# Kernel tuning notes

Measured on AMD Instinct MI355X. Metric: run time of the kernel, lower is better.

The kernel has to match this reference:

```python
import jax, jax.numpy as jnp
import numpy as np

E, K, H, I = 16, 4, 2048, 1024
B, S = 1, 2048


def setup_inputs() -> dict:
    key = jax.random.key(0)
    ks = jax.random.split(key, 5)
    scale_in = 1.0 / np.sqrt(H)
    scale_mid = 1.0 / np.sqrt(I)
    return {
        "x": jax.random.normal(ks[0], (B, S, H), dtype=jnp.float32),
        "gate_w": jax.random.normal(ks[1], (E, H), dtype=jnp.float32) * scale_in,
        "w1_gate": jax.random.normal(ks[2], (E, I, H), dtype=jnp.float32) * scale_in,
        "w1_up": jax.random.normal(ks[3], (E, I, H), dtype=jnp.float32) * scale_in,
        "w2": jax.random.normal(ks[4], (E, H, I), dtype=jnp.float32) * scale_mid,
        "topk": K,
    }


def reference(x, gate_w, w1_gate, w1_up, w2, topk):
    orig_shape = x.shape
    xt = x.reshape(-1, x.shape[-1])            # [T, H]
    T = xt.shape[0]
    n_exp = gate_w.shape[0]

    # Router: top-k logits, softmax over the selected k (as in the torch code).
    logits = xt @ gate_w.T                      # [T, E]
    topk_vals, topk_ids = jax.lax.top_k(logits, topk)
    topk_w = jax.nn.softmax(topk_vals, axis=-1)  # [T, K]

    # Dense per-token-per-expert combine weight; 0 for unselected experts.
    # Mathematically identical to the gather/scatter-add loop: unselected
    # experts contribute expert_out * 0.
    gate_dense = jnp.zeros((T, n_exp), dtype=xt.dtype)
    gate_dense = gate_dense.at[jnp.arange(T)[:, None], topk_ids].add(topk_w)

    # SwiGLU per expert (dense over experts; weights zero-out unused ones).
    g = jnp.einsum("th,eih->tei", xt, w1_gate)   # [T, E, I]
    u = jnp.einsum("th,eih->tei", xt, w1_up)     # [T, E, I]
    h = jax.nn.silu(g) * u                        # [T, E, I]
    out = jnp.einsum("tei,te,ehi->th", h, gate_dense, w2)  # [T, H]
    return out.reshape(orig_shape)
```

## Files before the change

kernel.cpp:

```cpp
#include <hip/hip_runtime.h>
#include <hip/hip_bf16.h>
#include <stdint.h>

#define NEXP 16
#define KSEL 4
#define HDIM 2048
#define IDIM 1024
#define TTOK 2048
#define MAXTILES 80
#define NTA 8
#define NTB 16
#define MAXBA (MAXTILES * NTA)
#define MAXBB (MAXTILES * NTB)

typedef __attribute__((ext_vector_type(8))) short bf16x8;
typedef __attribute__((ext_vector_type(4))) float f32x4;
typedef __attribute__((ext_vector_type(4))) unsigned int u32x4;
typedef unsigned int u32;

__device__ __forceinline__ uint32_t pack2(float a, float b) {
  __hip_bfloat162 h = __float22bfloat162_rn(float2{a, b});
  uint32_t u;
  __builtin_memcpy(&u, &h, 4);
  return u;
}
__device__ __forceinline__ ushort bf1(float a) {
  __hip_bfloat16 h = __float2bfloat16(a);
  ushort u;
  __builtin_memcpy(&u, &h, 2);
  return u;
}
__device__ __forceinline__ float bf2f(ushort u) {
  uint32_t v = (uint32_t)u << 16;
  float f;
  __builtin_memcpy(&f, &v, 4);
  return f;
}
__device__ __forceinline__ void gload16(const void* g, void* l) {
  __builtin_amdgcn_global_load_lds(
      (const __attribute__((address_space(1))) u32*)g,
      (__attribute__((address_space(3))) u32*)l, 16, 0, 0);
}
__device__ __forceinline__ int swzread(int row, int q) {
  return row * 32 + ((q ^ ((row >> 1) & 3)) << 3);
}

__global__ __launch_bounds__(256) void cvtw_kernel(
    const float* __restrict__ src, ushort* __restrict__ dst, int n8)
{
  const int stride = gridDim.x * 256;
  for (int i = blockIdx.x * 256 + threadIdx.x; i < n8; i += stride) {
    f32x4 a = __builtin_nontemporal_load(((const f32x4*)src) + i * 2);
    f32x4 b = __builtin_nontemporal_load(((const f32x4*)src) + i * 2 + 1);
    uint4 t;
    t.x = pack2(a[0], a[1]); t.y = pack2(a[2], a[3]);
    t.z = pack2(b[0], b[1]); t.w = pack2(b[2], b[3]);
    ((uint4*)dst)[i] = t;
  }
}

__global__ __launch_bounds__(256) void router_kernel(
    const float* __restrict__ x, const float* __restrict__ gw,
    ushort* __restrict__ xb, int* __restrict__ topk_id,
    float* __restrict__ topk_w)
{
  const int wid = threadIdx.x >> 6;
  const int lane = threadIdx.x & 63;
  const int t = blockIdx.x * 4 + wid;
  const float4* x4 = (const float4*)(x + (size_t)t * HDIM);
  const float4* gw4 = (const float4*)gw;
  float acc[NEXP];
#pragma unroll
  for (int e = 0; e < NEXP; ++e) acc[e] = 0.f;
#pragma unroll
  for (int i = 0; i < HDIM / 256; ++i) {
    const int idx = i * 64 + lane;
    float4 xv = x4[idx];
    uint2 xp;
    xp.x = pack2(xv.x, xv.y);
    xp.y = pack2(xv.z, xv.w);
    *(uint2*)(xb + (size_t)t * HDIM + idx * 4) = xp;
#pragma unroll
    for (int e = 0; e < NEXP; ++e) {
      float4 wv = gw4[e * (HDIM / 4) + idx];
      acc[e] += xv.x * wv.x + xv.y * wv.y + xv.z * wv.z + xv.w * wv.w;
    }
  }
#pragma unroll
  for (int e = 0; e < NEXP; ++e) {
#pragma unroll
    for (int off = 32; off >= 1; off >>= 1)
      acc[e] += __shfl_xor(acc[e], off);
  }
  if (lane == 0) {
    unsigned taken = 0;
    float vals[KSEL];
    int ids[KSEL];
#pragma unroll
    for (int k = 0; k < KSEL; ++k) {
      float bv = -3.4e38f; int bi = 0;
      for (int e = 0; e < NEXP; ++e)
        if (!((taken >> e) & 1u) && acc[e] > bv) { bv = acc[e]; bi = e; }
      taken |= 1u << bi; vals[k] = bv; ids[k] = bi;
    }
    float m = vals[0], s = 0.f, w[KSEL];
#pragma unroll
    for (int k = 0; k < KSEL; ++k) { w[k] = __expf(vals[k] - m); s += w[k]; }
    float is = 1.f / s;
#pragma unroll
    for (int k = 0; k < KSEL; ++k) {
      topk_id[t * KSEL + k] = ids[k];
      topk_w[t * KSEL + k] = w[k] * is;
    }
  }
}

__global__ __launch_bounds__(1024) void plan_scatter_kernel(
    const int* __restrict__ topk_id, int* __restrict__ counts,
    int* __restrict__ offsets, int* __restrict__ nWA, int* __restrict__ nWB,
    int* __restrict__ wlA, int* __restrict__ wlB,
    int* __restrict__ rowTok, int* __restrict__ inv)
{
  __shared__ int cnt[NEXP], off[NEXP], cur[NEXP], tiles[NEXP], pre[NEXP];
  const int tid = threadIdx.x;
  if (tid < NEXP) { cnt[tid] = 0; cur[tid] = 0; }
  __syncthreads();
  for (int i = tid; i < TTOK * KSEL; i += 1024)
    atomicAdd(&cnt[topk_id[i]], 1);
  __syncthreads();
  if (tid == 0) {
    int s = 0, p = 0;
    for (int e = 0; e < NEXP; ++e) {
      off[e] = s; s += cnt[e];
      tiles[e] = (cnt[e] + 127) >> 7;
      pre[e] = p; p += tiles[e];
    }
    *nWA = p * NTA;
    *nWB = p * NTB;
  }
  __syncthreads();
  if (tid < NEXP) {
    counts[tid] = cnt[tid];
    offsets[tid] = off[tid];
    const int e = tid, T = tiles[e];
    int idx = pre[e] * NTA;
    for (int nt = 0; nt < NTA; ++nt)
      for (int mt = 0; mt < T; ++mt)
        wlA[idx++] = (e << 12) | (nt << 6) | mt;
  } else if (tid < 2 * NEXP) {
    const int e = tid - NEXP, T = tiles[e];
    int idx = pre[e] * NTB;
    for (int nt = 0; nt < NTB; ++nt)
      for (int mt = 0; mt < T; ++mt)
        wlB[idx++] = (e << 12) | (nt << 6) | mt;
  }
  for (int i = tid; i < TTOK * KSEL; i += 1024) {
    const int e = topk_id[i];
    const int pos = atomicAdd(&cur[e], 1);
    const int row = off[e] + pos;
    rowTok[row] = i >> 2;
    inv[i] = row;
  }
}

__global__ __launch_bounds__(256) void gemmA_kernel(
    const ushort* __restrict__ xb, const ushort* __restrict__ wb,
    const int* __restrict__ rowTok, const int* __restrict__ counts,
    const int* __restrict__ offsets, const int* __restrict__ nW,
    const int* __restrict__ wl, ushort* __restrict__ outb)
{
  const int nTot = *nW;
  const int L = (blockIdx.x & 7) * (MAXBA / 8) + (blockIdx.x >> 3);
  if (L >= nTot) return;
  const int w = wl[L];
  const int e = w >> 12, nt = (w >> 6) & 63, mt = w & 63;
  const int n_e = counts[e], rowbase = offsets[e];

  __shared__ ushort As[2][128 * 32];
  __shared__ ushort Bs[2][128 * 32];

  const int tid = threadIdx.x;
  const int r0 = tid >> 2;
  const int ck = tid & 3;
  const int sch = (ck ^ ((r0 >> 1) & 3)) << 3;

  const int ar0 = mt * 128 + r0, ar1 = ar0 + 64;
  const int tok0 = rowTok[rowbase + (ar0 < n_e ? ar0 : n_e - 1)];
  const int tok1 = rowTok[rowbase + (ar1 < n_e ? ar1 : n_e - 1)];
  const ushort* pA0 = xb + (size_t)tok0 * HDIM + sch;
  const ushort* pA1 = xb + (size_t)tok1 * HDIM + sch;
  const size_t wbase = (size_t)e * IDIM * HDIM;
  const ushort* pB0 = wb + wbase + (size_t)(nt * 128 + r0) * HDIM + sch;
  const ushort* pB1 = wb + wbase + (size_t)(nt * 128 + r0 + 64) * HDIM + sch;

  const int lane = tid & 63;
  const int wid = tid >> 6;
  const int wr = (wid >> 1) << 6;
  const int wc = (wid & 1) << 6;
  const int lr = lane & 15;
  const int q = lane >> 4;

  f32x4 acc[4][4];
#pragma unroll
  for (int i = 0; i < 4; ++i)
#pragma unroll
    for (int j = 0; j < 4; ++j) acc[i][j] = (f32x4){0.f, 0.f, 0.f, 0.f};

  auto STAGE = [&](int b) {
    gload16(pA0, &As[b][tid * 8]);
    gload16(pA1, &As[b][2048 + tid * 8]);
    gload16(pB0, &Bs[b][tid * 8]);
    gload16(pB1, &Bs[b][2048 + tid * 8]);
    pA0 += 32; pA1 += 32; pB0 += 32; pB1 += 32;
  };

  const int NTK = HDIM / 32;
  STAGE(0);
  __syncthreads();
  int buf = 0;
  for (int kt = 0; kt < NTK; ++kt) {
    if (kt + 1 < NTK) STAGE(buf ^ 1);
    bf16x8 af[4], bfr[4];
#pragma unroll
    for (int mi = 0; mi < 4; ++mi)
      af[mi] = *(const bf16x8*)&As[buf][swzread(wr + mi * 16 + lr, q)];
#pragma unroll
    for (int ni = 0; ni < 4; ++ni)
      bfr[ni] = *(const bf16x8*)&Bs[buf][swzread(wc + ni * 16 + lr, q)];
#pragma unroll
    for (int mi = 0; mi < 4; ++mi)
#pragma unroll
      for (int ni = 0; ni < 4; ++ni)
        acc[mi][ni] = __builtin_amdgcn_mfma_f32_16x16x32_bf16(af[mi], bfr[ni], acc[mi][ni], 0, 0, 0);
    __syncthreads();
    buf ^= 1;
  }

#pragma unroll
  for (int mi = 0; mi < 4; ++mi) {
#pragma unroll
    for (int ni = 0; ni < 4; ++ni) {
      const int col = nt * 128 + wc + ni * 16 + lr;
#pragma unroll
      for (int r = 0; r < 4; ++r) {
        const int mrow = mt * 128 + wr + mi * 16 + q * 4 + r;
        if (mrow < n_e)
          outb[(size_t)(rowbase + mrow) * IDIM + col] = bf1(acc[mi][ni][r]);
      }
    }
  }
}

__global__ __launch_bounds__(256) void gemmB_kernel(
    const ushort* __restrict__ hb, const ushort* __restrict__ wb,
    const int* __restrict__ counts, const int* __restrict__ offsets,
    const int* __restrict__ nW, const int* __restrict__ wl,
    ushort* __restrict__ po)
{
  const int nTot = *nW;
  const int L = (blockIdx.x & 7) * (MAXBB / 8) + (blockIdx.x >> 3);
  if (L >= nTot) return;
  const int w = wl[L];
  const int e = w >> 12, nt = (w >> 6) & 63, mt = w & 63;
  const int n_e = counts[e], rowbase = offsets[e];

  __shared__ ushort As[2][128 * 32];
  __shared__ ushort Bs[2][128 * 32];

  const int tid = threadIdx.x;
  const int r0 = tid >> 2;
  const int ck = tid & 3;
  const int sch = (ck ^ ((r0 >> 1) & 3)) << 3;

  const int ar0 = mt * 128 + r0, ar1 = ar0 + 64;
  const int g0 = rowbase + (ar0 < n_e ? ar0 : n_e - 1);
  const int g1 = rowbase + (ar1 < n_e ? ar1 : n_e - 1);
  const ushort* pA0 = hb + (size_t)g0 * IDIM + sch;
  const ushort* pA1 = hb + (size_t)g1 * IDIM + sch;
  const size_t wbase = (size_t)e * HDIM * IDIM;
  const ushort* pB0 = wb + wbase + (size_t)(nt * 128 + r0) * IDIM + sch;
  const ushort* pB1 = wb + wbase + (size_t)(nt * 128 + r0 + 64) * IDIM + sch;

  const int lane = tid & 63;
  const int wid = tid >> 6;
  const int wr = (wid >> 1) << 6;
  const int wc = (wid & 1) << 6;
  const int lr = lane & 15;
  const int q = lane >> 4;

  f32x4 acc[4][4];
#pragma unroll
  for (int i = 0; i < 4; ++i)
#pragma unroll
    for (int j = 0; j < 4; ++j) acc[i][j] = (f32x4){0.f, 0.f, 0.f, 0.f};

  auto STAGE = [&](int b) {
    gload16(pA0, &As[b][tid * 8]);
    gload16(pA1, &As[b][2048 + tid * 8]);
    gload16(pB0, &Bs[b][tid * 8]);
    gload16(pB1, &Bs[b][2048 + tid * 8]);
    pA0 += 32; pA1 += 32; pB0 += 32; pB1 += 32;
  };

  const int NTK = IDIM / 32;
  STAGE(0);
  __syncthreads();
  int buf = 0;
  for (int kt = 0; kt < NTK; ++kt) {
    if (kt + 1 < NTK) STAGE(buf ^ 1);
    bf16x8 af[4], bfr[4];
#pragma unroll
    for (int mi = 0; mi < 4; ++mi)
      af[mi] = *(const bf16x8*)&As[buf][swzread(wr + mi * 16 + lr, q)];
#pragma unroll
    for (int ni = 0; ni < 4; ++ni)
      bfr[ni] = *(const bf16x8*)&Bs[buf][swzread(wc + ni * 16 + lr, q)];
#pragma unroll
    for (int mi = 0; mi < 4; ++mi)
#pragma unroll
      for (int ni = 0; ni < 4; ++ni)
        acc[mi][ni] = __builtin_amdgcn_mfma_f32_16x16x32_bf16(af[mi], bfr[ni], acc[mi][ni], 0, 0, 0);
    __syncthreads();
    buf ^= 1;
  }

#pragma unroll
  for (int mi = 0; mi < 4; ++mi) {
#pragma unroll
    for (int ni = 0; ni < 4; ++ni) {
      const int col = nt * 128 + wc + ni * 16 + lr;
#pragma unroll
      for (int r = 0; r < 4; ++r) {
        const int mrow = mt * 128 + wr + mi * 16 + q * 4 + r;
        if (mrow < n_e)
          po[(size_t)(rowbase + mrow) * HDIM + col] = bf1(acc[mi][ni][r]);
      }
    }
  }
}

__global__ __launch_bounds__(256) void silu_kernel(
    const ushort* __restrict__ g, const ushort* __restrict__ u,
    ushort* __restrict__ h, int n8)
{
  const int stride = gridDim.x * 256;
  for (int i = blockIdx.x * 256 + threadIdx.x; i < n8; i += stride) {
    u32x4 gv = __builtin_nontemporal_load(((const u32x4*)g) + i);
    u32x4 uv = __builtin_nontemporal_load(((const u32x4*)u) + i);
    uint4 hv;
#pragma unroll
    for (int wd = 0; wd < 4; ++wd) {
      const uint32_t gw2 = gv[wd], uw2 = uv[wd];
      const float g0 = bf2f((ushort)(gw2 & 0xffff));
      const float g1 = bf2f((ushort)(gw2 >> 16));
      const float u0 = bf2f((ushort)(uw2 & 0xffff));
      const float u1 = bf2f((ushort)(uw2 >> 16));
      const float h0 = (g0 / (1.f + __expf(-g0))) * u0;
      const float h1 = (g1 / (1.f + __expf(-g1))) * u1;
      (&hv.x)[wd] = pack2(h0, h1);
    }
    ((uint4*)h)[i] = hv;
  }
}

__global__ __launch_bounds__(256) void combine_kernel(
    const ushort* __restrict__ po, const int* __restrict__ inv,
    const float* __restrict__ tw, float* __restrict__ out)
{
  const int t = blockIdx.x;
  const int r0 = inv[t * 4 + 0], r1 = inv[t * 4 + 1];
  const int r2 = inv[t * 4 + 2], r3 = inv[t * 4 + 3];
  const float w0 = tw[t * 4 + 0], w1 = tw[t * 4 + 1];
  const float w2v = tw[t * 4 + 2], w3 = tw[t * 4 + 3];
  const int i = threadIdx.x;
  uint4 v0 = *(const uint4*)(po + (size_t)r0 * HDIM + i * 8);
  uint4 v1 = *(const uint4*)(po + (size_t)r1 * HDIM + i * 8);
  uint4 v2 = *(const uint4*)(po + (size_t)r2 * HDIM + i * 8);
  uint4 v3 = *(const uint4*)(po + (size_t)r3 * HDIM + i * 8);
  float o[8];
#pragma unroll
  for (int w = 0; w < 4; ++w) {
    const uint32_t a = (&v0.x)[w], b = (&v1.x)[w], c = (&v2.x)[w], d = (&v3.x)[w];
    o[w * 2 + 0] = w0 * __builtin_bit_cast(float, a << 16) +
                   w1 * __builtin_bit_cast(float, b << 16) +
                   w2v * __builtin_bit_cast(float, c << 16) +
                   w3 * __builtin_bit_cast(float, d << 16);
    o[w * 2 + 1] = w0 * __builtin_bit_cast(float, a & 0xffff0000u) +
                   w1 * __builtin_bit_cast(float, b & 0xffff0000u) +
                   w2v * __builtin_bit_cast(float, c & 0xffff0000u) +
                   w3 * __builtin_bit_cast(float, d & 0xffff0000u);
  }
  float4* o4 = (float4*)(out + (size_t)t * HDIM + i * 8);
  o4[0] = (float4){o[0], o[1], o[2], o[3]};
  o4[1] = (float4){o[4], o[5], o[6], o[7]};
}

extern "C" void kernel_launch(void* const* d_in, const int* in_sizes, int n_in,
                              void* d_out, int out_size, void* d_ws, size_t ws_size,
                              hipStream_t stream) {
  const float* x   = (const float*)d_in[0];
  const float* gw  = (const float*)d_in[1];
  const float* w1g = (const float*)d_in[2];
  const float* w1u = (const float*)d_in[3];
  const float* w2  = (const float*)d_in[4];
  float* out = (float*)d_out;

  char* ws = (char*)d_ws;
  ushort* xb   = (ushort*)(ws + 0);
  ushort* wbuf = (ushort*)(ws + 8388608);
  ushort* gbuf = (ushort*)(ws + 75497472);
  ushort* ubuf = (ushort*)(ws + 92274688);
  ushort* hbuf = (ushort*)(ws + 109051904);
  ushort* po   = (ushort*)(ws + 125829120);
  int*    tkid   = (int*)(ws + 159383552);
  float*  tkw    = (float*)(ws + 159383552 + 32768);
  int*    rowTok = (int*)(ws + 159383552 + 65536);
  int*    inv    = (int*)(ws + 159383552 + 98304);
  int*    ctrl   = (int*)(ws + 159514624);
  int* counts  = ctrl;
  int* offsets = ctrl + 32;
  int* nWA     = ctrl + 50;
  int* nWB     = ctrl + 51;
  int* wlA     = ctrl + 64;
  int* wlB     = ctrl + 64 + MAXBA;

  const int NW8 = (NEXP * IDIM * HDIM) / 8;

  router_kernel<<<TTOK / 4, 256, 0, stream>>>(x, gw, xb, tkid, tkw);
  plan_scatter_kernel<<<1, 1024, 0, stream>>>(tkid, counts, offsets, nWA, nWB,
                                              wlA, wlB, rowTok, inv);
  cvtw_kernel<<<2048, 256, 0, stream>>>(w1g, wbuf, NW8);
  gemmA_kernel<<<MAXBA, 256, 0, stream>>>(xb, wbuf, rowTok, counts, offsets,
                                          nWA, wlA, gbuf);
  cvtw_kernel<<<2048, 256, 0, stream>>>(w1u, wbuf, NW8);
  gemmA_kernel<<<MAXBA, 256, 0, stream>>>(xb, wbuf, rowTok, counts, offsets,
                                          nWA, wlA, ubuf);
  silu_kernel<<<2048, 256, 0, stream>>>(gbuf, ubuf, hbuf, (TTOK * KSEL * IDIM) / 8);
  cvtw_kernel<<<2048, 256, 0, stream>>>(w2, wbuf, NW8);
  gemmB_kernel<<<MAXBB, 256, 0, stream>>>(hbuf, wbuf, counts, offsets,
                                          nWB, wlB, po);
  combine_kernel<<<TTOK, 256, 0, stream>>>(po, inv, tkw, out);
}
```

Baseline: 376.1 us.

## Triple-buffer LDS staging in expert GEMMs with partial vmcnt waits

Both grouped GEMM kernels move from double to triple LDS buffers. Global-to-LDS loads are issued two k-tiles ahead, and the full __syncthreads is replaced by s_waitcnt vmcnt(4) plus a raw s_barrier, so the loads for the next tile can stay in flight across the barrier. The aim is to hide global memory latency behind MFMA work. In exchange, LDS use rises to 48KB per block, which may lower occupancy. Correctness depends on the hand-written wait counts matching the four loads issued per stage.

```diff
diff --git a/kernel.cpp b/kernel.cpp
--- a/kernel.cpp
+++ b/kernel.cpp
@@ -176,8 +176,8 @@
   const int e = w >> 12, nt = (w >> 6) & 63, mt = w & 63;
   const int n_e = counts[e], rowbase = offsets[e];
 
-  __shared__ ushort As[2][128 * 32];
-  __shared__ ushort Bs[2][128 * 32];
+  __shared__ ushort As[3][128 * 32];
+  __shared__ ushort Bs[3][128 * 32];
 
   const int tid = threadIdx.x;
   const int r0 = tid >> 2;
@@ -216,10 +216,13 @@
 
   const int NTK = HDIM / 32;
   STAGE(0);
-  __syncthreads();
+  STAGE(1);
+  asm volatile("s_waitcnt vmcnt(4)" ::: "memory");
+  __builtin_amdgcn_s_barrier();
+  __builtin_amdgcn_sched_barrier(0);
   int buf = 0;
   for (int kt = 0; kt < NTK; ++kt) {
-    if (kt + 1 < NTK) STAGE(buf ^ 1);
+    if (kt + 2 < NTK) STAGE(buf == 0 ? 2 : buf - 1);
     bf16x8 af[4], bfr[4];
 #pragma unroll
     for (int mi = 0; mi < 4; ++mi)
@@ -232,8 +235,15 @@
 #pragma unroll
       for (int ni = 0; ni < 4; ++ni)
         acc[mi][ni] = __builtin_amdgcn_mfma_f32_16x16x32_bf16(af[mi], bfr[ni], acc[mi][ni], 0, 0, 0);
-    __syncthreads();
-    buf ^= 1;
+    if (kt + 1 < NTK) {
+      if (kt + 2 < NTK)
+        asm volatile("s_waitcnt vmcnt(4)" ::: "memory");
+      else
+        asm volatile("s_waitcnt vmcnt(0)" ::: "memory");
+      __builtin_amdgcn_s_barrier();
+      __builtin_amdgcn_sched_barrier(0);
+    }
+    buf = (buf == 2) ? 0 : buf + 1;
   }
 
 #pragma unroll
@@ -264,8 +274,8 @@
   const int e = w >> 12, nt = (w >> 6) & 63, mt = w & 63;
   const int n_e = counts[e], rowbase = offsets[e];
 
-  __shared__ ushort As[2][128 * 32];
-  __shared__ ushort Bs[2][128 * 32];
+  __shared__ ushort As[3][128 * 32];
+  __shared__ ushort Bs[3][128 * 32];
 
   const int tid = threadIdx.x;
   const int r0 = tid >> 2;
@@ -304,10 +314,13 @@
 
   const int NTK = IDIM / 32;
   STAGE(0);
-  __syncthreads();
+  STAGE(1);
+  asm volatile("s_waitcnt vmcnt(4)" ::: "memory");
+  __builtin_amdgcn_s_barrier();
+  __builtin_amdgcn_sched_barrier(0);
   int buf = 0;
   for (int kt = 0; kt < NTK; ++kt) {
-    if (kt + 1 < NTK) STAGE(buf ^ 1);
+    if (kt + 2 < NTK) STAGE(buf == 0 ? 2 : buf - 1);
     bf16x8 af[4], bfr[4];
 #pragma unroll
     for (int mi = 0; mi < 4; ++mi)
@@ -320,8 +333,15 @@
 #pragma unroll
       for (int ni = 0; ni < 4; ++ni)
         acc[mi][ni] = __builtin_amdgcn_mfma_f32_16x16x32_bf16(af[mi], bfr[ni], acc[mi][ni], 0, 0, 0);
-    __syncthreads();
-    buf ^= 1;
+    if (kt + 1 < NTK) {
+      if (kt + 2 < NTK)
+        asm volatile("s_waitcnt vmcnt(4)" ::: "memory");
+      else
+        asm volatile("s_waitcnt vmcnt(0)" ::: "memory");
+      __builtin_amdgcn_s_barrier();
+      __builtin_amdgcn_sched_barrier(0);
+    }
+    buf = (buf == 2) ? 0 : buf + 1;
   }
 
 #pragma unroll
```

Result: slower. 393.1 us (+4.5%).

## Overlap weight fp32-to-bf16 conversion with router and GEMM kernels via extra blocks

Applied to the files above, without the earlier changes.

Removes the three standalone weight-conversion launches. Each conversion is now done by extra blocks appended to the preceding kernel's grid: w1_gate during the router, w1_up during the first GEMM, and w2 during the second GEMM. Separate bf16 buffers are allocated per weight so they can be written while another is being read. The aim is to hide the memory-bound conversion behind compute-heavy GEMM work and cut launch gaps, at the cost of more workspace and of conversion blocks competing with GEMM blocks for bandwidth and CUs.

```diff
diff --git a/kernel.cpp b/kernel.cpp
--- a/kernel.cpp
+++ b/kernel.cpp
@@ -12,6 +12,8 @@
 #define NTB 16
 #define MAXBA (MAXTILES * NTA)
 #define MAXBB (MAXTILES * NTB)
+#define NCVT 1024
+#define NW8 ((NEXP * IDIM * HDIM) / 8)
 
 typedef __attribute__((ext_vector_type(8))) short bf16x8;
 typedef __attribute__((ext_vector_type(4))) float f32x4;
@@ -44,12 +46,11 @@
 __device__ __forceinline__ int swzread(int row, int q) {
   return row * 32 + ((q ^ ((row >> 1) & 3)) << 3);
 }
-
-__global__ __launch_bounds__(256) void cvtw_kernel(
-    const float* __restrict__ src, ushort* __restrict__ dst, int n8)
-{
-  const int stride = gridDim.x * 256;
-  for (int i = blockIdx.x * 256 + threadIdx.x; i < n8; i += stride) {
+__device__ __forceinline__ void cvt_body(const float* __restrict__ src,
+                                         ushort* __restrict__ dst,
+                                         int blk, int nblk) {
+  const int stride = nblk * 256;
+  for (int i = blk * 256 + (int)threadIdx.x; i < NW8; i += stride) {
     f32x4 a = __builtin_nontemporal_load(((const f32x4*)src) + i * 2);
     f32x4 b = __builtin_nontemporal_load(((const f32x4*)src) + i * 2 + 1);
     uint4 t;
@@ -62,8 +63,13 @@
 __global__ __launch_bounds__(256) void router_kernel(
     const float* __restrict__ x, const float* __restrict__ gw,
     ushort* __restrict__ xb, int* __restrict__ topk_id,
-    float* __restrict__ topk_w)
-{
+    float* __restrict__ topk_w, const float* __restrict__ cvsrc,
+    ushort* __restrict__ cvdst)
+{
+  if (blockIdx.x >= TTOK / 4) {
+    cvt_body(cvsrc, cvdst, blockIdx.x - TTOK / 4, NCVT);
+    return;
+  }
   const int wid = threadIdx.x >> 6;
   const int lane = threadIdx.x & 63;
   const int t = blockIdx.x * 4 + wid;
@@ -167,8 +173,13 @@
     const ushort* __restrict__ xb, const ushort* __restrict__ wb,
     const int* __restrict__ rowTok, const int* __restrict__ counts,
     const int* __restrict__ offsets, const int* __restrict__ nW,
-    const int* __restrict__ wl, ushort* __restrict__ outb)
-{
+    const int* __restrict__ wl, ushort* __restrict__ outb,
+    const float* __restrict__ cvsrc, ushort* __restrict__ cvdst)
+{
+  if (blockIdx.x >= MAXBA) {
+    cvt_body(cvsrc, cvdst, blockIdx.x - MAXBA, NCVT);
+    return;
+  }
   const int nTot = *nW;
   const int L = (blockIdx.x & 7) * (MAXBA / 8) + (blockIdx.x >> 3);
   if (L >= nTot) return;
@@ -406,17 +417,19 @@
   float* out = (float*)d_out;
 
   char* ws = (char*)d_ws;
-  ushort* xb   = (ushort*)(ws + 0);
-  ushort* wbuf = (ushort*)(ws + 8388608);
-  ushort* gbuf = (ushort*)(ws + 75497472);
-  ushort* ubuf = (ushort*)(ws + 92274688);
-  ushort* hbuf = (ushort*)(ws + 109051904);
-  ushort* po   = (ushort*)(ws + 125829120);
-  int*    tkid   = (int*)(ws + 159383552);
-  float*  tkw    = (float*)(ws + 159383552 + 32768);
-  int*    rowTok = (int*)(ws + 159383552 + 65536);
-  int*    inv    = (int*)(ws + 159383552 + 98304);
-  int*    ctrl   = (int*)(ws + 159514624);
+  ushort* xb    = (ushort*)(ws + 0);
+  ushort* wbufG = (ushort*)(ws + 8388608);
+  ushort* wbufU = (ushort*)(ws + 75497472);
+  ushort* wbuf2 = (ushort*)(ws + 142606336);
+  ushort* gbuf  = (ushort*)(ws + 209715200);
+  ushort* ubuf  = (ushort*)(ws + 226492416);
+  ushort* hbuf  = (ushort*)(ws + 243269632);
+  ushort* po    = (ushort*)(ws + 260046848);
+  int*    tkid   = (int*)(ws + 293601280);
+  float*  tkw    = (float*)(ws + 293601280 + 32768);
+  int*    rowTok = (int*)(ws + 293601280 + 65536);
+  int*    inv    = (int*)(ws + 293601280 + 98304);
+  int*    ctrl   = (int*)(ws + 293732352);
   int* counts  = ctrl;
   int* offsets = ctrl + 32;
   int* nWA     = ctrl + 50;
@@ -424,20 +437,18 @@
   int* wlA     = ctrl + 64;
   int* wlB     = ctrl + 64 + MAXBA;
 
-  const int NW8 = (NEXP * IDIM * HDIM) / 8;
-
-  router_kernel<<<TTOK / 4, 256, 0, stream>>>(x, gw, xb, tkid, tkw);
+  router_kernel<<<TTOK / 4 + NCVT, 256, 0, stream>>>(x, gw, xb, tkid, tkw,
+                                                     w1g, wbufG);
   plan_scatter_kernel<<<1, 1024, 0, stream>>>(tkid, counts, offsets, nWA, nWB,
                                               wlA, wlB, rowTok, inv);
-  cvtw_kernel<<<2048, 256, 0, stream>>>(w1g, wbuf, NW8);
-  gemmA_kernel<<<MAXBA, 256, 0, stream>>>(xb, wbuf, rowTok, counts, offsets,
-                                          nWA, wlA, gbuf);
-  cvtw_kernel<<<2048, 256, 0, stream>>>(w1u, wbuf, NW8);
-  gemmA_kernel<<<MAXBA, 256, 0, stream>>>(xb, wbuf, rowTok, counts, offsets,
-                                          nWA, wlA, ubuf);
+  gemmA_kernel<<<MAXBA + NCVT, 256, 0, stream>>>(xb, wbufG, rowTok, counts,
+                                                 offsets, nWA, wlA, gbuf,
+                                                 w1u, wbufU);
+  gemmA_kernel<<<MAXBA + NCVT, 256, 0, stream>>>(xb, wbufU, rowTok, counts,
+                                                 offsets, nWA, wlA, ubuf,
+                                                 w2, wbuf2);
   silu_kernel<<<2048, 256, 0, stream>>>(gbuf, ubuf, hbuf, (TTOK * KSEL * IDIM) / 8);
-  cvtw_kernel<<<2048, 256, 0, stream>>>(w2, wbuf, NW8);
-  gemmB_kernel<<<MAXBB, 256, 0, stream>>>(hbuf, wbuf, counts, offsets,
+  gemmB_kernel<<<MAXBB, 256, 0, stream>>>(hbuf, wbuf2, counts, offsets,
                                           nWB, wlB, po);
   combine_kernel<<<TTOK, 256, 0, stream>>>(po, inv, tkw, out);
 }
```

Result: faster. 350.0 us (-6.9%).
